# Optimization experiments

Measured on AMD Instinct MI355X. Metric: run time of the kernel, lower is better.

The kernel has to match this reference:

```python
import jax, jax.numpy as jnp
import numpy as np

B, T, C, H = 2, 2048, 1024, 16  # head_dim for V = C//H = 64; QK head dim = 3


def setup_inputs() -> dict:
    key = jax.random.key(0)
    ks = jax.random.split(key, 6)
    x = jax.random.normal(ks[0], (B, T, C), dtype=jnp.float32)
    wq = jax.random.normal(ks[1], (C, H * 3), dtype=jnp.float32) * (C ** -0.5)
    wk = jax.random.normal(ks[2], (C, H * 3), dtype=jnp.float32) * (C ** -0.5)
    wv = jax.random.normal(ks[3], (C, C), dtype=jnp.float32) * (C ** -0.5)
    wo = jax.random.normal(ks[4], (C, C), dtype=jnp.float32) * (C ** -0.5)
    dirs = jax.random.normal(ks[5], (H, 3), dtype=jnp.float32)
    head_dirs = dirs / jnp.linalg.norm(dirs, axis=1, keepdims=True)  # unit trigram dirs
    scale = jnp.full((1,), 1.0 / np.sqrt(3.0), dtype=jnp.float32)
    return {"x": x, "wq": wq, "wk": wk, "wv": wv, "wo": wo,
            "head_dirs": head_dirs, "scale": scale}


def reference(x, wq, wk, wv, wo, head_dirs, scale):
    b, t, c = x.shape
    h = head_dirs.shape[0]
    hd = c // h
    # projections: QK live in a 3-dim geometric space per head
    q3 = (x @ wq).reshape(b, t, h, 3).transpose(0, 2, 1, 3)   # (B,H,T,3)
    k3 = (x @ wk).reshape(b, t, h, 3).transpose(0, 2, 1, 3)   # (B,H,T,3)
    v = (x @ wv).reshape(b, t, h, hd).transpose(0, 2, 1, 3)   # (B,H,T,hd)
    # projections of q,k onto per-head trigram directions
    q_on_dir = jnp.einsum('bhtd,hd->bht', q3, head_dirs)      # (B,H,T)
    k_on_dir = jnp.einsum('bhtd,hd->bht', k3, head_dirs)      # (B,H,T)
    dot_scores = jnp.einsum('bhtd,bhsd->bhts', q3, k3) * scale  # (B,H,T,T)
    geo_bias = q_on_dir[..., :, None] * k_on_dir[..., None, :]  # outer product bias
    scores = dot_scores + geo_bias
    causal = jnp.tril(jnp.ones((t, t), dtype=bool))
    scores = jnp.where(causal, scores, -jnp.inf)
    attn = jax.nn.softmax(scores, axis=-1)  # dropout p=0 -> identity
    out = jnp.einsum('bhts,bhsd->bhtd', attn, v)
    out = out.transpose(0, 2, 1, 3).reshape(b, t, c)
    return out @ wo
```

## Files before the change

### kernel.cpp

```cpp
#include <hip/hip_runtime.h>
#include <hip/hip_bf16.h>


typedef short bf16x8 __attribute__((ext_vector_type(8)));
typedef float f32x4 __attribute__((ext_vector_type(4)));
typedef __hip_bfloat16 bf16_t;
typedef unsigned int __attribute__((address_space(1))) u32_as1;
typedef unsigned int __attribute__((address_space(3))) u32_as3;

#define T_SEQ 2048
#define NHEAD 16
#define CDIM 1024
#define L2E 1.4426950408889634f

__device__ __forceinline__ void gl_lds16(const void* g, void* l) {
  __builtin_amdgcn_global_load_lds((const u32_as1*)g, (u32_as3*)l, 16, 0, 0);
}

__device__ __forceinline__ f32x4 mfma16(bf16x8 a, bf16x8 b, f32x4 c) {
  return __builtin_amdgcn_mfma_f32_16x16x32_bf16(a, b, c, 0, 0, 0);
}

__device__ __forceinline__ unsigned short f2bf(float f) {
  __hip_bfloat16 h = __float2bfloat16(f);
  return *(unsigned short*)&h;
}

__device__ __forceinline__ float fast_exp2(float x) {
#if __has_builtin(__builtin_amdgcn_exp2f)
  return __builtin_amdgcn_exp2f(x);
#else
  return exp2f(x);
#endif
}

__global__ __launch_bounds__(256) void k_prep(const float* __restrict__ x,
                                              const float* __restrict__ wq,
                                              const float* __restrict__ wk,
                                              const float* __restrict__ wv,
                                              const float* __restrict__ wo,
                                              bf16_t* __restrict__ xb,
                                              bf16_t* __restrict__ wqkT,
                                              bf16_t* __restrict__ wvT,
                                              bf16_t* __restrict__ woT) {
  __shared__ bf16_t tile[32][33];
  int bid = blockIdx.x, tid = threadIdx.x;
  if (bid < 4096) {
    int i = bid * 256 + tid;
    float4 v = ((const float4*)x)[i];
    ushort4 o;
    o.x = f2bf(v.x); o.y = f2bf(v.y); o.z = f2bf(v.z); o.w = f2bf(v.w);
    ((ushort4*)xb)[i] = o;
    return;
  }
  const float* src; bf16_t* dst; int R, C, bx, by;
  if (bid < 5120)      { int t = bid - 4096; src = wv; dst = wvT;            R = 1024; C = 1024; bx = t & 31; by = t >> 5; }
  else if (bid < 6144) { int t = bid - 5120; src = wo; dst = woT;            R = 1024; C = 1024; bx = t & 31; by = t >> 5; }
  else if (bid < 6208) { int t = bid - 6144; src = wq; dst = wqkT;           R = 1024; C = 48;   bx = t & 1;  by = t >> 1; }
  else                 { int t = bid - 6208; src = wk; dst = wqkT + 48*1024; R = 1024; C = 48;   bx = t & 1;  by = t >> 1; }
  int tx = tid & 31, ty = tid >> 5;
  int r0 = by * 32, c0 = bx * 32;
#pragma unroll
  for (int j = 0; j < 32; j += 8) {
    int r = r0 + ty + j, c = c0 + tx;
    if (r < R && c < C) tile[ty + j][tx] = __float2bfloat16(src[(size_t)r * C + c]);
  }
  __syncthreads();
#pragma unroll
  for (int j = 0; j < 32; j += 8) {
    int c = c0 + ty + j, r = r0 + tx;
    if (r < R && c < C) dst[(size_t)c * R + r] = tile[tx][ty + j];
  }
}

__global__ __launch_bounds__(256) void k_gemmqk(const bf16_t* __restrict__ A,
                                                const bf16_t* __restrict__ Bt,
                                                void* __restrict__ Cout,
                                                int M, int N, int K, int mode,
                                                int nbx, int fuse_qk,
                                                const bf16_t* __restrict__ xb,
                                                const bf16_t* __restrict__ wqkT,
                                                const float* __restrict__ head_dirs,
                                                const float* __restrict__ scale,
                                                float* __restrict__ Qt,
                                                float* __restrict__ Kt) {
  __shared__ union SMem {
    struct {
      alignas(16) bf16_t A[2][2 * 64 * 32];
      alignas(16) bf16_t B[2][2 * 128 * 32];
    } g;
    float red[4][16][96];
  } sm;
  int tid = threadIdx.x, wave = tid >> 6, lane = tid & 63;
  int g = lane >> 4, li = lane & 15;

  if (fuse_qk && blockIdx.x < 256) {
    int m0 = blockIdx.x * 16;
    f32x4 acc[6] = {};
    int kb = wave * 256;
    for (int k0 = kb; k0 < kb + 256; k0 += 32) {
      bf16x8 a = *(const bf16x8*)(xb + (size_t)(m0 + li) * 1024 + k0 + g * 8);
#pragma unroll
      for (int nt = 0; nt < 6; ++nt) {
        bf16x8 bb = *(const bf16x8*)(wqkT + (size_t)(nt * 16 + li) * 1024 + k0 + g * 8);
        acc[nt] = mfma16(a, bb, acc[nt]);
      }
    }
#pragma unroll
    for (int nt = 0; nt < 6; ++nt)
#pragma unroll
      for (int r = 0; r < 4; ++r) sm.red[wave][g * 4 + r][nt * 16 + li] = acc[nt][r];
    __syncthreads();
    for (int i = tid; i < 16 * 96; i += 256) {
      int row = i / 96, col = i - (i / 96) * 96;
      float v = sm.red[0][row][col] + sm.red[1][row][col] + sm.red[2][row][col] + sm.red[3][row][col];
      if (col >= 48) {
        int n = col - 48;
        int h = n / 3, c = n - h * 3;
        int mg = m0 + row;
        int bb = mg >> 11, tt = mg & 2047;
        Kt[(((size_t)bb * NHEAD + h) * 3 + c) * T_SEQ + tt] = v;
      } else {
        sm.red[0][row][col] = v;
      }
    }
    __syncthreads();
    int row = tid >> 4, h = tid & 15;
    float q0 = sm.red[0][row][h * 3 + 0];
    float q1 = sm.red[0][row][h * 3 + 1];
    float q2 = sm.red[0][row][h * 3 + 2];
    float d0 = head_dirs[h * 3 + 0];
    float d1 = head_dirs[h * 3 + 1];
    float d2 = head_dirs[h * 3 + 2];
    float sc = scale[0] * L2E;
    float dot = (q0 * d0 + q1 * d1 + q2 * d2) * L2E;
    int mg = m0 + row;
    int bb = mg >> 11, tt = mg & 2047;
    size_t base = ((size_t)bb * NHEAD + h) * 3 * T_SEQ + tt;
    Qt[base] = sc * q0 + d0 * dot;
    Qt[base + T_SEQ] = sc * q1 + d1 * dot;
    Qt[base + 2 * T_SEQ] = sc * q2 + d2 * dot;
    return;
  }

  int gb = blockIdx.x - (fuse_qk ? 256 : 0);
  int bx = gb % nbx, by = gb / nbx;
  int n0 = bx * 128, m0 = by * 64;
  int wm = wave >> 1, wn = wave & 1;

  const bf16_t* gA0 = A + (size_t)(m0 + (tid >> 2)) * K + (tid & 3) * 8;
  const bf16_t* gB0 = Bt + (size_t)(n0 + (tid >> 2)) * K + (tid & 3) * 8;
  const bf16_t* gB1 = Bt + (size_t)(n0 + 64 + (tid >> 2)) * K + (tid & 3) * 8;

#define GSTAGE(bufi, kk)                                          \
  {                                                               \
    char* aB = (char*)&sm.g.A[bufi][0];                           \
    char* bB = (char*)&sm.g.B[bufi][0];                           \
    gl_lds16(gA0 + (kk), aB + tid * 16);                          \
    gl_lds16(gA0 + (kk) + 32, aB + (256 + tid) * 16);             \
    gl_lds16(gB0 + (kk), bB + tid * 16);                          \
    gl_lds16(gB1 + (kk), bB + (256 + tid) * 16);                  \
    gl_lds16(gB0 + (kk) + 32, bB + (512 + tid) * 16);             \
    gl_lds16(gB1 + (kk) + 32, bB + (768 + tid) * 16);             \
  }

  f32x4 acc[2][4] = {};
  GSTAGE(0, 0);

  for (int k0 = 0; k0 < K; k0 += 64) {
    int cur = (k0 >> 6) & 1;
    __syncthreads();
    if (k0 + 64 < K) GSTAGE(cur ^ 1, k0 + 64);
#pragma unroll
    for (int kk = 0; kk < 2; ++kk) {
      bf16x8 af[2], bfr[4];
#pragma unroll
      for (int mt = 0; mt < 2; ++mt)
        af[mt] = *(const bf16x8*)&sm.g.A[cur][kk * 2048 + (wm * 32 + mt * 16 + li) * 32 + g * 8];
#pragma unroll
      for (int nt = 0; nt < 4; ++nt)
        bfr[nt] = *(const bf16x8*)&sm.g.B[cur][kk * 4096 + (wn * 64 + nt * 16 + li) * 32 + g * 8];
#pragma unroll
      for (int mt = 0; mt < 2; ++mt)
#pragma unroll
        for (int nt = 0; nt < 4; ++nt)
          acc[mt][nt] = mfma16(af[mt], bfr[nt], acc[mt][nt]);
    }
  }
#undef GSTAGE

#pragma unroll
  for (int mt = 0; mt < 2; ++mt)
#pragma unroll
    for (int nt = 0; nt < 4; ++nt)
#pragma unroll
      for (int r = 0; r < 4; ++r) {
        int m = m0 + wm * 32 + mt * 16 + g * 4 + r;
        int n = n0 + wn * 64 + nt * 16 + li;
        float v = acc[mt][nt][r];
        if (mode == 0) {
          int bb = n >> 11, tt = n & 2047;
          ((bf16_t*)Cout)[((size_t)bb * 1024 + m) * T_SEQ + tt] = __float2bfloat16(v);
        } else {
          ((float*)Cout)[(size_t)m * N + n] = v;
        }
      }
}

__global__ __launch_bounds__(256, 4) void k_attn(const float* __restrict__ Qt,
                                                 const float* __restrict__ Kt,
                                                 const bf16_t* __restrict__ VT,
                                                 bf16_t* __restrict__ att) {
  __shared__ alignas(16) bf16_t Vb[2][2][64 * 64];
  __shared__ alignas(16) float Ks[2][3 * 128];
  int tid = threadIdx.x, wave = tid >> 6, lane = tid & 63;
  int g = lane >> 4, li = lane & 15;
  int bid = blockIdx.x;
  int p = bid >> 5, bh = bid & 31;
  int a = p & 7, bq = p >> 3;
  int qt = (bq == 0) ? a : (bq == 1) ? 31 - a : (bq == 2) ? 8 + a : 23 - a;
  int b = bh >> 4, h = bh & 15;
  int mw = wave * 16;

  const float* Qp = Qt + (size_t)bh * 3 * T_SEQ;
  const float* Kp = Kt + (size_t)bh * 3 * T_SEQ;
  const bf16_t* Vp = VT + (size_t)bh * 64 * T_SEQ;

  int tq = qt * 64 + mw + li;
  float q0 = Qp[tq], q1 = Qp[T_SEQ + tq], q2 = Qp[2 * T_SEQ + tq];

  bf16x8 bones;
  unsigned short ob = (li == 0) ? (unsigned short)0x3F80 : (unsigned short)0;
#pragma unroll
  for (int j = 0; j < 8; ++j) bones[j] = (short)ob;

  const bf16_t* vg[2];
#pragma unroll
  for (int pp = 0; pp < 2; ++pp) {
    int P = pp * 256 + wave * 64 + lane;
    int d = P >> 3, c = (P & 7) ^ (d & 7);
    vg[pp] = Vp + (size_t)d * T_SEQ + c * 8;
  }
  int kch = (wave == 3) ? lane : 32 + lane;
  const float* kg = Kp + (size_t)(kch >> 5) * T_SEQ + (kch & 31) * 4;
  int kbase = (wave == 3) ? 0 : 512;

#define STAGE(bufi, s0v)                                                      \
  {                                                                           \
    _Pragma("unroll") for (int sub_ = 0; sub_ < 2; ++sub_)                    \
        _Pragma("unroll") for (int p_ = 0; p_ < 2; ++p_)                      \
            gl_lds16(vg[p_] + (s0v) + sub_ * 64,                              \
                     (char*)&Vb[bufi][sub_][0] + (p_ * 256 + wave * 64) * 16);\
    if (wave >= 2) gl_lds16(kg + (s0v), (char*)&Ks[bufi][0] + kbase);         \
  }

#define BUILD_AFRAG(MASKED)                                                   \
  _Pragma("unroll") for (int half = 0; half < 2; ++half) {                    \
    int kb = sub * 64 + half * 32 + g * 8;                                    \
    f32x4 kv[3][2];                                                           \
    _Pragma("unroll") for (int c = 0; c < 3; ++c) {                           \
      kv[c][0] = *(const f32x4*)(ks + c * 128 + kb);                          \
      kv[c][1] = *(const f32x4*)(ks + c * 128 + kb + 4);                      \
    }                                                                         \
    _Pragma("unroll") for (int j = 0; j < 8; ++j) {                           \
      float scv = q0 * kv[0][j >> 2][j & 3] + q1 * kv[1][j >> 2][j & 3] +     \
                  q2 * kv[2][j >> 2][j & 3];                                  \
      float pv = fast_exp2(fminf(scv, 115.4f));                               \
      if (MASKED && (bkg + half * 32 + g * 8 + j > tq)) pv = 0.0f;            \
      afrag[half][j] = (short)f2bf(pv);                                       \
    }                                                                         \
  }

  int NT = (qt + 2) >> 1;
  STAGE(0, 0);

  f32x4 acc[5] = {};
  int sw = li & 7;
  int qmin = qt * 64 + mw;
  int qmax = qmin + 15;

  for (int st = 0; st < NT; ++st) {
    int buf = st & 1;
    __syncthreads();
    if (st + 1 < NT) STAGE(buf ^ 1, (st + 1) * 128);
    const float* ks = &Ks[buf][0];
#pragma unroll
    for (int sub = 0; sub < 2; ++sub) {
      int bkg = st * 128 + sub * 64;
      if (bkg > qmax) continue;
      bf16x8 afrag[2];
      if (bkg + 63 > qmin) { BUILD_AFRAG(1) } else { BUILD_AFRAG(0) }
      const bf16_t* vb = &Vb[buf][sub][0];
#pragma unroll
      for (int nt = 0; nt < 4; ++nt) {
        int row = nt * 16 + li;
        bf16x8 b0 = *(const bf16x8*)&vb[row * 64 + (g ^ sw) * 8];
        bf16x8 b1 = *(const bf16x8*)&vb[row * 64 + ((4 + g) ^ sw) * 8];
        acc[nt] = mfma16(afrag[0], b0, acc[nt]);
        acc[nt] = mfma16(afrag[1], b1, acc[nt]);
      }
      acc[4] = mfma16(afrag[0], bones, acc[4]);
      acc[4] = mfma16(afrag[1], bones, acc[4]);
    }
  }
#undef STAGE
#undef BUILD_AFRAG

  float linv[4];
#pragma unroll
  for (int r = 0; r < 4; ++r)
    linv[r] = 1.0f / fmaxf(__shfl(acc[4][r], lane & 48), 1e-35f);

#pragma unroll
  for (int nt = 0; nt < 4; ++nt)
#pragma unroll
    for (int r = 0; r < 4; ++r) {
      int t = qt * 64 + mw + g * 4 + r;
      att[((size_t)b * T_SEQ + t) * CDIM + h * 64 + nt * 16 + li] =
          __float2bfloat16(acc[nt][r] * linv[r]);
    }
}

extern "C" void kernel_launch(void* const* d_in, const int* in_sizes, int n_in,
                              void* d_out, int out_size, void* d_ws, size_t ws_size,
                              hipStream_t stream) {
  const float* x  = (const float*)d_in[0];
  const float* wq = (const float*)d_in[1];
  const float* wk = (const float*)d_in[2];
  const float* wv = (const float*)d_in[3];
  const float* wo = (const float*)d_in[4];
  const float* hd = (const float*)d_in[5];
  const float* sc = (const float*)d_in[6];
  float* out = (float*)d_out;

  char* ws = (char*)d_ws;
  bf16_t* wqkT = (bf16_t*)(ws + 0);
  bf16_t* wvT  = (bf16_t*)(ws + 196608);
  bf16_t* woT  = (bf16_t*)(ws + 2293760);
  float*  Qt   = (float*)(ws + 4390912);
  float*  Kt   = (float*)(ws + 5177344);
  bf16_t* VT   = (bf16_t*)(ws + 5963776);
  bf16_t* att  = (bf16_t*)(ws + 14352384);
  bf16_t* xb   = (bf16_t*)(ws + 22740992);

  k_prep<<<6272, 256, 0, stream>>>(x, wq, wk, wv, wo, xb, wqkT, wvT, woT);

  k_gemmqk<<<768, 256, 0, stream>>>(wvT, xb, VT, 1024, 4096, 1024, 0, 32, 1,
                                    xb, wqkT, hd, sc, Qt, Kt);

  k_attn<<<1024, 256, 0, stream>>>(Qt, Kt, VT, att);

  k_gemmqk<<<512, 256, 0, stream>>>(att, woT, out, 4096, 1024, 1024, 1, 8, 0,
                                    nullptr, nullptr, nullptr, nullptr, nullptr, nullptr);
}
```

Baseline: 151.2 us.

## Read K and V directly from global memory in attention, dropping LDS staging

```diff
diff --git a/kernel.cpp b/kernel.cpp
--- a/kernel.cpp
+++ b/kernel.cpp
@@ -211,8 +211,6 @@
                                                  const float* __restrict__ Kt,
                                                  const bf16_t* __restrict__ VT,
                                                  bf16_t* __restrict__ att) {
-  __shared__ alignas(16) bf16_t Vb[2][2][64 * 64];
-  __shared__ alignas(16) float Ks[2][3 * 128];
   int tid = threadIdx.x, wave = tid >> 6, lane = tid & 63;
   int g = lane >> 4, li = lane & 15;
   int bid = blockIdx.x;
@@ -234,76 +232,40 @@
 #pragma unroll
   for (int j = 0; j < 8; ++j) bones[j] = (short)ob;
 
-  const bf16_t* vg[2];
-#pragma unroll
-  for (int pp = 0; pp < 2; ++pp) {
-    int P = pp * 256 + wave * 64 + lane;
-    int d = P >> 3, c = (P & 7) ^ (d & 7);
-    vg[pp] = Vp + (size_t)d * T_SEQ + c * 8;
-  }
-  int kch = (wave == 3) ? lane : 32 + lane;
-  const float* kg = Kp + (size_t)(kch >> 5) * T_SEQ + (kch & 31) * 4;
-  int kbase = (wave == 3) ? 0 : 512;
-
-#define STAGE(bufi, s0v)                                                      \
-  {                                                                           \
-    _Pragma("unroll") for (int sub_ = 0; sub_ < 2; ++sub_)                    \
-        _Pragma("unroll") for (int p_ = 0; p_ < 2; ++p_)                      \
-            gl_lds16(vg[p_] + (s0v) + sub_ * 64,                              \
-                     (char*)&Vb[bufi][sub_][0] + (p_ * 256 + wave * 64) * 16);\
-    if (wave >= 2) gl_lds16(kg + (s0v), (char*)&Ks[bufi][0] + kbase);         \
-  }
-
 #define BUILD_AFRAG(MASKED)                                                   \
   _Pragma("unroll") for (int half = 0; half < 2; ++half) {                    \
-    int kb = sub * 64 + half * 32 + g * 8;                                    \
+    const float* kp = Kp + s64 * 64 + half * 32 + g * 8;                      \
     f32x4 kv[3][2];                                                           \
     _Pragma("unroll") for (int c = 0; c < 3; ++c) {                           \
-      kv[c][0] = *(const f32x4*)(ks + c * 128 + kb);                          \
-      kv[c][1] = *(const f32x4*)(ks + c * 128 + kb + 4);                      \
+      kv[c][0] = *(const f32x4*)(kp + c * T_SEQ);                             \
+      kv[c][1] = *(const f32x4*)(kp + c * T_SEQ + 4);                         \
     }                                                                         \
     _Pragma("unroll") for (int j = 0; j < 8; ++j) {                           \
       float scv = q0 * kv[0][j >> 2][j & 3] + q1 * kv[1][j >> 2][j & 3] +     \
                   q2 * kv[2][j >> 2][j & 3];                                  \
       float pv = fast_exp2(fminf(scv, 115.4f));                               \
-      if (MASKED && (bkg + half * 32 + g * 8 + j > tq)) pv = 0.0f;            \
+      if (MASKED && (s64 * 64 + half * 32 + g * 8 + j > tq)) pv = 0.0f;       \
       afrag[half][j] = (short)f2bf(pv);                                       \
     }                                                                         \
   }
 
-  int NT = (qt + 2) >> 1;
-  STAGE(0, 0);
-
   f32x4 acc[5] = {};
-  int sw = li & 7;
-  int qmin = qt * 64 + mw;
-  int qmax = qmin + 15;
-
-  for (int st = 0; st < NT; ++st) {
-    int buf = st & 1;
-    __syncthreads();
-    if (st + 1 < NT) STAGE(buf ^ 1, (st + 1) * 128);
-    const float* ks = &Ks[buf][0];
-#pragma unroll
-    for (int sub = 0; sub < 2; ++sub) {
-      int bkg = st * 128 + sub * 64;
-      if (bkg > qmax) continue;
-      bf16x8 afrag[2];
-      if (bkg + 63 > qmin) { BUILD_AFRAG(1) } else { BUILD_AFRAG(0) }
-      const bf16_t* vb = &Vb[buf][sub][0];
-#pragma unroll
-      for (int nt = 0; nt < 4; ++nt) {
-        int row = nt * 16 + li;
-        bf16x8 b0 = *(const bf16x8*)&vb[row * 64 + (g ^ sw) * 8];
-        bf16x8 b1 = *(const bf16x8*)&vb[row * 64 + ((4 + g) ^ sw) * 8];
-        acc[nt] = mfma16(afrag[0], b0, acc[nt]);
-        acc[nt] = mfma16(afrag[1], b1, acc[nt]);
-      }
-      acc[4] = mfma16(afrag[0], bones, acc[4]);
-      acc[4] = mfma16(afrag[1], bones, acc[4]);
-    }
-  }
-#undef STAGE
+
+  for (int s64 = 0; s64 <= qt; ++s64) {
+    bf16x8 afrag[2];
+    if (s64 == qt) { BUILD_AFRAG(1) } else { BUILD_AFRAG(0) }
+    const bf16_t* vb = Vp + (size_t)s64 * 64;
+#pragma unroll
+    for (int nt = 0; nt < 4; ++nt) {
+      const bf16_t* vrow = vb + (size_t)(nt * 16 + li) * T_SEQ;
+      bf16x8 b0 = *(const bf16x8*)(vrow + g * 8);
+      bf16x8 b1 = *(const bf16x8*)(vrow + 32 + g * 8);
+      acc[nt] = mfma16(afrag[0], b0, acc[nt]);
+      acc[nt] = mfma16(afrag[1], b1, acc[nt]);
+    }
+    acc[4] = mfma16(afrag[0], bones, acc[4]);
+    acc[4] = mfma16(afrag[1], bones, acc[4]);
+  }
 #undef BUILD_AFRAG
 
   float linv[4];
```

Measured after the change: 202.4 us. 33.9% more time.
